# Kernel tuning notes

Measured on AMD Instinct MI355X. Metric: run time of the kernel, lower is better.

## Reference

```python
import jax, jax.numpy as jnp
import numpy as np

B, NBAND, C, T = 2, 40, 64, 1500
NUM_CODE = 1024


def setup_inputs() -> dict:
    key = jax.random.key(0)
    k1, k2 = jax.random.split(key)
    x = jax.random.normal(k1, (B, NBAND, C, T), dtype=jnp.float32)
    # layer_idx == 0 init: unit-norm codes per band
    cb = jax.random.normal(k2, (NBAND, NUM_CODE, C), dtype=jnp.float32)
    eps = jnp.finfo(jnp.float32).eps
    cb = cb / jnp.sqrt(jnp.sum(cb * cb, axis=-1, keepdims=True) + eps)
    return {"x": x, "codebook": cb}


def reference(x, codebook):
    batch, nband, nchan, time = x.shape
    num_code = codebook.shape[1]
    # x.detach().permute(0,3,1,2).view(B*T, nband, nchan)
    xd = jax.lax.stop_gradient(x).transpose(0, 3, 1, 2).reshape(batch * time, nband, nchan)
    dist = (
        jnp.sum(xd * xd, axis=-1, keepdims=True)
        + jnp.sum(codebook * codebook, axis=-1)
        - 2.0 * jnp.einsum("nbc,bkc->nbk", xd, codebook)
    )
    min_idx = jnp.argmin(dist, axis=-1)  # [BT, nband]
    # per-band gather: quantized[n, b] = codebook[b, min_idx[n, b]]
    quantized = codebook[jnp.arange(nband)[None, :], min_idx]  # [BT, nband, nchan]
    # view(B, T, nband, nchan).permute(0,2,3,1)
    return quantized.reshape(batch, time, nband, nchan).transpose(0, 2, 3, 1)
```

## Files before the change

### kernel.cpp

```cpp
#include <hip/hip_runtime.h>


#define NBAND  40
#define CH     64
#define TT     1500
#define NCODE  1024
#define MT     64
#define NTILE  24
#define PAD    68
#define THRESH 1e-3f

typedef short v8s __attribute__((ext_vector_type(8)));
typedef float v4f __attribute__((ext_vector_type(4)));

#define CBF_USHORTS ((size_t)NBAND * 32 * 8 * 64 * 8)
#define CBF_BYTES   (CBF_USHORTS * 2)
#define WS_NEEDED   (CBF_BYTES + (size_t)NBAND * NCODE * 4)

__device__ __forceinline__ unsigned short f2bf(float f) {
    unsigned u = __float_as_uint(f);
    return (unsigned short)((u + 0x7FFFu + ((u >> 16) & 1u)) >> 16);
}
__device__ __forceinline__ float bf2f(unsigned short h) {
    return __uint_as_float(((unsigned)h) << 16);
}
__device__ __forceinline__ unsigned ford(float f) {
    unsigned u = __float_as_uint(f);
    return (u & 0x80000000u) ? ~u : (u | 0x80000000u);
}
__device__ __forceinline__ unsigned long long packsk(float f, unsigned k) {
    return ((unsigned long long)ford(f) << 32) | (unsigned long long)k;
}
__device__ __forceinline__ float med3f(float a, float b, float c) {
#if __has_builtin(__builtin_amdgcn_fmed3f)
    return __builtin_amdgcn_fmed3f(a, b, c);
#else
    return fminf(fmaxf(a, b), c);
#endif
}

typedef __attribute__((address_space(1))) const unsigned char* gas_p;
typedef __attribute__((address_space(3))) unsigned char*       las_p;
__device__ __forceinline__ void async_ld16(const void* g, void* l) {
    __builtin_amdgcn_global_load_lds((gas_p)g, (las_p)l, 16, 0, 0);
}

__global__ __launch_bounds__(256)
void vq_prep(const float* __restrict__ cb,
             unsigned short* __restrict__ CBF,
             float* __restrict__ C2) {
    const int id     = blockIdx.x;
    const int v      = id >> 3;
    const int band   = (id & 7) + 8 * (v % 5);
    const int gchunk = v / 5;
    const int g      = gchunk * 4 + (threadIdx.x >> 6);
    const int lane   = threadIdx.x & 63;
    const int col    = lane & 15;
    const int quad   = lane >> 4;

    float sq[2] = {0.f, 0.f};
    #pragma unroll
    for (int l = 0; l < 4; ++l) {
        const int ni = l >> 1, ks = l & 1;
        const int code = g * 32 + ni * 16 + col;
        const int c0   = ks * 32 + quad * 8;
        const float* src = cb + ((size_t)(band * NCODE + code)) * CH + c0;
        const float4 v0 = *(const float4*)src;
        const float4 v1 = *(const float4*)(src + 4);
        const float vv[8] = {v0.x, v0.y, v0.z, v0.w, v1.x, v1.y, v1.z, v1.w};
        union { unsigned short u[8]; v8s v; } hh, ll;
        #pragma unroll
        for (int j = 0; j < 8; ++j) {
            const unsigned short h = f2bf(vv[j]);
            hh.u[j] = h;
            ll.u[j] = f2bf(vv[j] - bf2f(h));
            sq[ni] = fmaf(vv[j], vv[j], sq[ni]);
        }
        const size_t gb = (size_t)(band * 32 + g) * 8;
        *(v8s*)&CBF[(gb + l)     * 512 + lane * 8] = hh.v;
        *(v8s*)&CBF[(gb + 4 + l) * 512 + lane * 8] = ll.v;
    }
    #pragma unroll
    for (int ni = 0; ni < 2; ++ni) {
        sq[ni] += __shfl_xor(sq[ni], 16);
        sq[ni] += __shfl_xor(sq[ni], 32);
    }
    if (quad == 0) {
        C2[band * NCODE + g * 32 + col]      = sq[0];
        C2[band * NCODE + g * 32 + 16 + col] = sq[1];
    }
}

__global__ __launch_bounds__(256, 4)
void vq_main(const float* __restrict__ x,
             const float* __restrict__ cb,
             const unsigned short* __restrict__ CBF,
             const float* __restrict__ C2f,
             float* __restrict__ out) {
    __shared__ alignas(16) unsigned char SMEM[32768];
    __shared__ float c2_s[NCODE];
    __shared__ unsigned long long best_s[MT];
    __shared__ unsigned amb_s[2];
    __shared__ float xrow_s[CH];

    const int id    = blockIdx.x;
    const int v     = id >> 3;
    const int band  = (id & 7) + 8 * (v % 5);
    const int tb    = v / 5;
    const int tile  = tb % NTILE;
    const int batch = tb / NTILE;
    const int t0    = tile * MT;

    const int tid   = threadIdx.x;
    const int wave  = tid >> 6;
    const int lane  = tid & 63;
    const int quad  = lane >> 4;
    const int col   = lane & 15;
    const int thalf = wave & 1;
    const int khalf = wave >> 1;

    if (tid < 2) amb_s[tid] = 0u;
    {
        const float* src = C2f + band * NCODE;
        #pragma unroll
        for (int i = 0; i < 4; ++i) c2_s[tid + 256 * i] = src[tid + 256 * i];
    }
    {
        unsigned short* XH_s = (unsigned short*)SMEM;
        unsigned short* XL_s = XH_s + MT * PAD;
        const int c = tid & 63;
        const int g = tid >> 6;
        const float* src = x + ((size_t)(batch * NBAND + band) * CH + c) * TT + t0;
        #pragma unroll
        for (int i = 0; i < 4; ++i) {
            const int t = (g + 4 * i) * 4;
            float4 v4 = make_float4(0.f, 0.f, 0.f, 0.f);
            if (t0 + t + 3 < TT) v4 = *(const float4*)(src + t);
            const float vv[4] = {v4.x, v4.y, v4.z, v4.w};
            #pragma unroll
            for (int j = 0; j < 4; ++j) {
                const unsigned short h = f2bf(vv[j]);
                XH_s[(t + j) * PAD + c] = h;
                XL_s[(t + j) * PAD + c] = f2bf(vv[j] - bf2f(h));
            }
        }
    }
    __syncthreads();

    v8s ah[2][2], al[2][2];
    {
        unsigned short* XH_s = (unsigned short*)SMEM;
        unsigned short* XL_s = XH_s + MT * PAD;
        #pragma unroll
        for (int mi = 0; mi < 2; ++mi)
            #pragma unroll
            for (int ks = 0; ks < 2; ++ks) {
                const int off = (thalf * 32 + mi * 16 + col) * PAD + ks * 32 + quad * 8;
                ah[mi][ks] = *(const v8s*)&XH_s[off];
                al[mi][ks] = *(const v8s*)&XL_s[off];
            }
    }
    __syncthreads();

    float m1[8], m2[8];
    int   id8[8];
    #pragma unroll
    for (int i = 0; i < 8; ++i) { m1[i] = 3.4028235e38f; m2[i] = 3.4028235e38f; id8[i] = 0x7fffffff; }

    unsigned short* LBUF = (unsigned short*)SMEM;
    const unsigned short* cbase = CBF + (size_t)(band * 32) * 4096 + (size_t)lane * 8;
    const int pbase = thalf * 4;

    auto stage_round = [&](int r, int b) {
        const int group = khalf * 16 + r;
        #pragma unroll
        for (int i = 0; i < 4; ++i) {
            const int p = pbase + i;
            async_ld16(cbase + (size_t)group * 4096 + p * 512,
                       LBUF + (size_t)b * 8192 + khalf * 4096 + p * 512);
        }
    };

    stage_round(0, 0);

    for (int r = 0; r < 16; ++r) {
        __syncthreads();
        if (r + 1 < 16) stage_round(r + 1, (r + 1) & 1);

        const unsigned short* lb = LBUF + (size_t)(r & 1) * 8192 + khalf * 4096 + lane * 8;
        v4f acc[2][2];
        #pragma unroll
        for (int mi = 0; mi < 2; ++mi)
            #pragma unroll
            for (int ni = 0; ni < 2; ++ni) acc[mi][ni] = (v4f){0.f, 0.f, 0.f, 0.f};

        #pragma unroll
        for (int ks = 0; ks < 2; ++ks) {
            const v8s bh0 = *(const v8s*)(lb + (0 + ks) * 512);
            const v8s bh1 = *(const v8s*)(lb + (2 + ks) * 512);
            const v8s bl0 = *(const v8s*)(lb + (4 + ks) * 512);
            const v8s bl1 = *(const v8s*)(lb + (6 + ks) * 512);
            #pragma unroll
            for (int mi = 0; mi < 2; ++mi) {
                acc[mi][0] = __builtin_amdgcn_mfma_f32_16x16x32_bf16(ah[mi][ks], bh0, acc[mi][0], 0, 0, 0);
                acc[mi][1] = __builtin_amdgcn_mfma_f32_16x16x32_bf16(ah[mi][ks], bh1, acc[mi][1], 0, 0, 0);
            }
            #pragma unroll
            for (int mi = 0; mi < 2; ++mi) {
                acc[mi][0] = __builtin_amdgcn_mfma_f32_16x16x32_bf16(ah[mi][ks], bl0, acc[mi][0], 0, 0, 0);
                acc[mi][1] = __builtin_amdgcn_mfma_f32_16x16x32_bf16(ah[mi][ks], bl1, acc[mi][1], 0, 0, 0);
            }
            #pragma unroll
            for (int mi = 0; mi < 2; ++mi) {
                acc[mi][0] = __builtin_amdgcn_mfma_f32_16x16x32_bf16(al[mi][ks], bh0, acc[mi][0], 0, 0, 0);
                acc[mi][1] = __builtin_amdgcn_mfma_f32_16x16x32_bf16(al[mi][ks], bh1, acc[mi][1], 0, 0, 0);
            }
        }
        #pragma unroll
        for (int ni = 0; ni < 2; ++ni) {
            const int   kg  = khalf * 512 + r * 32 + ni * 16 + col;
            const float c2v = c2_s[kg];
            #pragma unroll
            for (int mi = 0; mi < 2; ++mi)
                #pragma unroll
                for (int rr = 0; rr < 4; ++rr) {
                    const int j = mi * 4 + rr;
                    const float s = fmaf(-2.f, acc[mi][ni][rr], c2v);
                    m2[j] = med3f(s, m1[j], m2[j]);
                    const bool lt = s < m1[j];
                    m1[j]  = lt ? s : m1[j];
                    id8[j] = lt ? kg : id8[j];
                }
        }
    }
    __syncthreads();

    float* RM1 = (float*)SMEM;
    float* RM2 = RM1 + MT * 32;
    int*   RI  = (int*)(RM2 + MT * 32);
    #pragma unroll
    for (int j = 0; j < 8; ++j) {
        const int t    = thalf * 32 + (j >> 2) * 16 + quad * 4 + (j & 3);
        const int slot = khalf * 16 + col;
        RM1[t * 32 + slot] = m1[j];
        RM2[t * 32 + slot] = m2[j];
        RI [t * 32 + slot] = id8[j];
    }
    __syncthreads();

    if (tid < MT) {
        const int t = tid;
        float M1 = RM1[t * 32], M2 = RM2[t * 32];
        int   I  = RI[t * 32];
        #pragma unroll 8
        for (int j = 1; j < 32; ++j) {
            const float a1 = RM1[t * 32 + j];
            const float a2 = RM2[t * 32 + j];
            const int   ai = RI [t * 32 + j];
            if (a1 < M1 || (a1 == M1 && ai < I)) { M2 = fminf(M2, M1); M1 = a1; I = ai; }
            else                                  { M2 = fminf(M2, a1); }
            M2 = fminf(M2, a2);
        }
        best_s[t] = packsk(M1, (unsigned)I);
        if ((M2 - M1) <= THRESH && t0 + t < TT)
            atomicOr(&amb_s[t >> 5], 1u << (t & 31));
    }
    __syncthreads();

    for (int t = 0; t < MT; ++t) {
        if ((amb_s[t >> 5] >> (t & 31)) & 1u) {
            if (tid < CH) xrow_s[tid] = x[((size_t)(batch * NBAND + band) * CH + tid) * TT + t0 + t];
            if (tid == CH) best_s[t] = ~0ULL;
            __syncthreads();
            #pragma unroll
            for (int i = 0; i < 4; ++i) {
                const int k = tid * 4 + i;
                const float* crow = cb + ((size_t)(band * NCODE + k)) * CH;
                float dot = 0.f, c2e = 0.f;
                #pragma unroll 8
                for (int c = 0; c < CH; ++c) {
                    const float cv = crow[c];
                    dot = fmaf(cv, xrow_s[c], dot);
                    c2e = fmaf(cv, cv, c2e);
                }
                atomicMin(&best_s[t], packsk(fmaf(-2.f, dot, c2e), (unsigned)k));
            }
            __syncthreads();
        }
    }
    __syncthreads();

    {
        float* OT = (float*)SMEM;
        #pragma unroll
        for (int rr = 0; rr < MT; rr += 4) {
            const int row = rr + wave;
            const unsigned idx = (unsigned)(best_s[row] & 0xFFFFFFFFull) & (NCODE - 1);
            OT[row * 67 + lane] = cb[((size_t)(band * NCODE + idx)) * CH + lane];
        }
        __syncthreads();
        const int tloc = tid & 63;
        const int cq   = tid >> 6;
        if (t0 + tloc < TT) {
            float* ob = out + ((size_t)(batch * NBAND + band) * CH) * TT + t0 + tloc;
            #pragma unroll
            for (int i = 0; i < 16; ++i) {
                const int c = cq * 16 + i;
                ob[(size_t)c * TT] = OT[tloc * 67 + c];
            }
        }
    }
}

#define TN 128
#define KC 128
__global__ __launch_bounds__(256, 2)
void vq_fp32_kernel(const float* __restrict__ x,
                    const float* __restrict__ cb,
                    float* __restrict__ out) {
    __shared__ float XT_s[CH * TN];
    __shared__ float CBT_s[CH * KC];
    __shared__ float c2part[256];
    const int tile = blockIdx.x, band = blockIdx.y, batch = blockIdx.z;
    const int t0 = tile * TN;
    const int tid = threadIdx.x;
    const int tx = tid & 15, ty = tid >> 4;
    {
        const int c = tid >> 2, q = tid & 3;
        const float* src = x + ((size_t)(batch * NBAND + band) * CH + c) * TT + t0;
        #pragma unroll
        for (int i = 0; i < 8; ++i) {
            const int t = q * 32 + i * 4;
            float4 v = make_float4(0.f, 0.f, 0.f, 0.f);
            if (t0 + t < TT) v = *(const float4*)(src + t);
            *(float4*)&XT_s[c * TN + t] = v;
        }
    }
    float vmin[8]; int vidx[8];
    #pragma unroll
    for (int i = 0; i < 8; ++i) { vmin[i] = 3.4e38f; vidx[i] = 0x7fffffff; }
    for (int kc = 0; kc < NCODE; kc += KC) {
        __syncthreads();
        {
            const int k = tid >> 1, ch0 = (tid & 1) * 32;
            const float* src = cb + ((size_t)(band * NCODE + kc + k)) * CH + ch0;
            float s = 0.f;
            #pragma unroll
            for (int i = 0; i < 8; ++i) {
                const float4 v = *(const float4*)(src + i * 4);
                const int c0 = ch0 + i * 4;
                CBT_s[(c0 + 0) * KC + k] = v.x; CBT_s[(c0 + 1) * KC + k] = v.y;
                CBT_s[(c0 + 2) * KC + k] = v.z; CBT_s[(c0 + 3) * KC + k] = v.w;
                s = fmaf(v.x, v.x, s); s = fmaf(v.y, v.y, s);
                s = fmaf(v.z, v.z, s); s = fmaf(v.w, v.w, s);
            }
            c2part[tid] = s;
        }
        __syncthreads();
        float acc[8][8];
        #pragma unroll
        for (int ii = 0; ii < 8; ++ii)
            #pragma unroll
            for (int jj = 0; jj < 8; ++jj) acc[ii][jj] = 0.f;
        #pragma unroll 4
        for (int c = 0; c < CH; ++c) {
            const float4 xa0 = *(const float4*)&XT_s[c * TN + tx * 4];
            const float4 xa1 = *(const float4*)&XT_s[c * TN + 64 + tx * 4];
            const float4 cv0 = *(const float4*)&CBT_s[c * KC + ty * 4];
            const float4 cv1 = *(const float4*)&CBT_s[c * KC + 64 + ty * 4];
            const float xa[8] = {xa0.x, xa0.y, xa0.z, xa0.w, xa1.x, xa1.y, xa1.z, xa1.w};
            const float cv[8] = {cv0.x, cv0.y, cv0.z, cv0.w, cv1.x, cv1.y, cv1.z, cv1.w};
            #pragma unroll
            for (int ii = 0; ii < 8; ++ii)
                #pragma unroll
                for (int jj = 0; jj < 8; ++jj) acc[ii][jj] = fmaf(xa[ii], cv[jj], acc[ii][jj]);
        }
        #pragma unroll
        for (int jj = 0; jj < 8; ++jj) {
            const int kl = (jj < 4) ? (ty * 4 + jj) : (64 + ty * 4 + (jj - 4));
            const float c2v = c2part[2 * kl] + c2part[2 * kl + 1];
            const int kglob = kc + kl;
            #pragma unroll
            for (int ii = 0; ii < 8; ++ii) {
                const float score = fmaf(-2.f, acc[ii][jj], c2v);
                if (score < vmin[ii]) { vmin[ii] = score; vidx[ii] = kglob; }
            }
        }
    }
    __syncthreads();
    float* redv = XT_s;
    int* redi = (int*)(XT_s + TN * 16);
    int* idxs = (int*)(XT_s + TN * 32);
    #pragma unroll
    for (int ii = 0; ii < 8; ++ii) {
        const int t = (ii < 4) ? (tx * 4 + ii) : (64 + tx * 4 + (ii - 4));
        redv[t * 16 + ty] = vmin[ii];
        redi[t * 16 + ty] = vidx[ii];
    }
    __syncthreads();
    if (tid < TN) {
        float bv = redv[tid * 16]; int bi = redi[tid * 16];
        #pragma unroll
        for (int j = 1; j < 16; ++j) {
            const float v = redv[tid * 16 + j]; const int id = redi[tid * 16 + j];
            if (v < bv || (v == bv && id < bi)) { bv = v; bi = id; }
        }
        idxs[tid] = bi;
    }
    __syncthreads();
    {
        const int tloc = tid & 127, chalf = tid >> 7;
        if (t0 + tloc < TT) {
            const int idx = idxs[tloc];
            const float* crow = cb + ((size_t)(band * NCODE + idx)) * CH;
            float* ob = out + ((size_t)(batch * NBAND + band) * CH) * TT + t0 + tloc;
            #pragma unroll
            for (int i = 0; i < 32; ++i) {
                const int c = chalf * 32 + i;
                ob[(size_t)c * TT] = crow[c];
            }
        }
    }
}

extern "C" void kernel_launch(void* const* d_in, const int* in_sizes, int n_in,
                              void* d_out, int out_size, void* d_ws, size_t ws_size,
                              hipStream_t stream) {
    const float* x  = (const float*)d_in[0];
    const float* cb = (const float*)d_in[1];
    float* out = (float*)d_out;
    if (ws_size >= WS_NEEDED) {
        unsigned short* CBF = (unsigned short*)d_ws;
        float* C2 = (float*)((char*)d_ws + CBF_BYTES);
        vq_prep<<<dim3(8 * 5 * 8), dim3(256), 0, stream>>>(cb, CBF, C2);
        vq_main<<<dim3(8 * 5 * NTILE * 2), dim3(256), 0, stream>>>(x, cb, CBF, C2, out);
    } else {
        dim3 grid((TT + TN - 1) / TN, NBAND, 2);
        vq_fp32_kernel<<<grid, dim3(256), 0, stream>>>(x, cb, out);
    }
}
```

Baseline: 194.2 us.

## Double time tile to 128 rows and reduce argmin with wave shuffles

Measured after the change: 215.7 us. 1.11x slower.

```diff
diff --git a/kernel.cpp b/kernel.cpp
--- a/kernel.cpp
+++ b/kernel.cpp
@@ -5,8 +5,8 @@
 #define CH     64
 #define TT     1500
 #define NCODE  1024
-#define MT     64
-#define NTILE  24
+#define MT     128
+#define NTILE  12
 #define PAD    68
 #define THRESH 1e-3f
 
@@ -27,6 +27,9 @@
 __device__ __forceinline__ unsigned ford(float f) {
     unsigned u = __float_as_uint(f);
     return (u & 0x80000000u) ? ~u : (u | 0x80000000u);
+}
+__device__ __forceinline__ float finv(unsigned u) {
+    return (u & 0x80000000u) ? __uint_as_float(u & 0x7FFFFFFFu) : __uint_as_float(~u);
 }
 __device__ __forceinline__ unsigned long long packsk(float f, unsigned k) {
     return ((unsigned long long)ford(f) << 32) | (unsigned long long)k;
@@ -91,16 +94,18 @@
     }
 }
 
-__global__ __launch_bounds__(256, 4)
+__global__ __launch_bounds__(256, 3)
 void vq_main(const float* __restrict__ x,
              const float* __restrict__ cb,
              const unsigned short* __restrict__ CBF,
              const float* __restrict__ C2f,
              float* __restrict__ out) {
-    __shared__ alignas(16) unsigned char SMEM[32768];
+    __shared__ alignas(16) unsigned char SMEM[MT * PAD * 2 * 2];
     __shared__ float c2_s[NCODE];
     __shared__ unsigned long long best_s[MT];
-    __shared__ unsigned amb_s[2];
+    __shared__ unsigned long long MB_s[MT * 2];
+    __shared__ float MS_s[MT * 2];
+    __shared__ unsigned amb_s[4];
     __shared__ float xrow_s[CH];
 
     const int id    = blockIdx.x;
@@ -119,7 +124,7 @@
     const int thalf = wave & 1;
     const int khalf = wave >> 1;
 
-    if (tid < 2) amb_s[tid] = 0u;
+    if (tid < 4) amb_s[tid] = 0u;
     {
         const float* src = C2f + band * NCODE;
         #pragma unroll
@@ -132,7 +137,7 @@
         const int g = tid >> 6;
         const float* src = x + ((size_t)(batch * NBAND + band) * CH + c) * TT + t0;
         #pragma unroll
-        for (int i = 0; i < 4; ++i) {
+        for (int i = 0; i < 8; ++i) {
             const int t = (g + 4 * i) * 4;
             float4 v4 = make_float4(0.f, 0.f, 0.f, 0.f);
             if (t0 + t + 3 < TT) v4 = *(const float4*)(src + t);
@@ -147,25 +152,25 @@
     }
     __syncthreads();
 
-    v8s ah[2][2], al[2][2];
+    v8s ah[4][2], al[4][2];
     {
         unsigned short* XH_s = (unsigned short*)SMEM;
         unsigned short* XL_s = XH_s + MT * PAD;
         #pragma unroll
-        for (int mi = 0; mi < 2; ++mi)
+        for (int mi = 0; mi < 4; ++mi)
             #pragma unroll
             for (int ks = 0; ks < 2; ++ks) {
-                const int off = (thalf * 32 + mi * 16 + col) * PAD + ks * 32 + quad * 8;
+                const int off = (thalf * 64 + mi * 16 + col) * PAD + ks * 32 + quad * 8;
                 ah[mi][ks] = *(const v8s*)&XH_s[off];
                 al[mi][ks] = *(const v8s*)&XL_s[off];
             }
     }
     __syncthreads();
 
-    float m1[8], m2[8];
-    int   id8[8];
-    #pragma unroll
-    for (int i = 0; i < 8; ++i) { m1[i] = 3.4028235e38f; m2[i] = 3.4028235e38f; id8[i] = 0x7fffffff; }
+    float m1[16], m2[16];
+    int   id16[16];
+    #pragma unroll
+    for (int i = 0; i < 16; ++i) { m1[i] = 3.4028235e38f; m2[i] = 3.4028235e38f; id16[i] = 0x7fffffff; }
 
     unsigned short* LBUF = (unsigned short*)SMEM;
     const unsigned short* cbase = CBF + (size_t)(band * 32) * 4096 + (size_t)lane * 8;
@@ -188,82 +193,73 @@
         if (r + 1 < 16) stage_round(r + 1, (r + 1) & 1);
 
         const unsigned short* lb = LBUF + (size_t)(r & 1) * 8192 + khalf * 4096 + lane * 8;
-        v4f acc[2][2];
-        #pragma unroll
-        for (int mi = 0; mi < 2; ++mi)
-            #pragma unroll
-            for (int ni = 0; ni < 2; ++ni) acc[mi][ni] = (v4f){0.f, 0.f, 0.f, 0.f};
-
-        #pragma unroll
-        for (int ks = 0; ks < 2; ++ks) {
-            const v8s bh0 = *(const v8s*)(lb + (0 + ks) * 512);
-            const v8s bh1 = *(const v8s*)(lb + (2 + ks) * 512);
-            const v8s bl0 = *(const v8s*)(lb + (4 + ks) * 512);
-            const v8s bl1 = *(const v8s*)(lb + (6 + ks) * 512);
-            #pragma unroll
-            for (int mi = 0; mi < 2; ++mi) {
-                acc[mi][0] = __builtin_amdgcn_mfma_f32_16x16x32_bf16(ah[mi][ks], bh0, acc[mi][0], 0, 0, 0);
-                acc[mi][1] = __builtin_amdgcn_mfma_f32_16x16x32_bf16(ah[mi][ks], bh1, acc[mi][1], 0, 0, 0);
-            }
-            #pragma unroll
-            for (int mi = 0; mi < 2; ++mi) {
-                acc[mi][0] = __builtin_amdgcn_mfma_f32_16x16x32_bf16(ah[mi][ks], bl0, acc[mi][0], 0, 0, 0);
-                acc[mi][1] = __builtin_amdgcn_mfma_f32_16x16x32_bf16(ah[mi][ks], bl1, acc[mi][1], 0, 0, 0);
-            }
-            #pragma unroll
-            for (int mi = 0; mi < 2; ++mi) {
-                acc[mi][0] = __builtin_amdgcn_mfma_f32_16x16x32_bf16(al[mi][ks], bh0, acc[mi][0], 0, 0, 0);
-                acc[mi][1] = __builtin_amdgcn_mfma_f32_16x16x32_bf16(al[mi][ks], bh1, acc[mi][1], 0, 0, 0);
-            }
-        }
         #pragma unroll
         for (int ni = 0; ni < 2; ++ni) {
+            v4f acc[4];
+            #pragma unroll
+            for (int mi = 0; mi < 4; ++mi) acc[mi] = (v4f){0.f, 0.f, 0.f, 0.f};
+            #pragma unroll
+            for (int ks = 0; ks < 2; ++ks) {
+                const v8s bh = *(const v8s*)(lb + (ni * 2 + ks) * 512);
+                #pragma unroll
+                for (int mi = 0; mi < 4; ++mi)
+                    acc[mi] = __builtin_amdgcn_mfma_f32_16x16x32_bf16(ah[mi][ks], bh, acc[mi], 0, 0, 0);
+                #pragma unroll
+                for (int mi = 0; mi < 4; ++mi)
+                    acc[mi] = __builtin_amdgcn_mfma_f32_16x16x32_bf16(al[mi][ks], bh, acc[mi], 0, 0, 0);
+                const v8s bl = *(const v8s*)(lb + (4 + ni * 2 + ks) * 512);
+                #pragma unroll
+                for (int mi = 0; mi < 4; ++mi)
+                    acc[mi] = __builtin_amdgcn_mfma_f32_16x16x32_bf16(ah[mi][ks], bl, acc[mi], 0, 0, 0);
+            }
             const int   kg  = khalf * 512 + r * 32 + ni * 16 + col;
             const float c2v = c2_s[kg];
             #pragma unroll
-            for (int mi = 0; mi < 2; ++mi)
+            for (int mi = 0; mi < 4; ++mi)
                 #pragma unroll
                 for (int rr = 0; rr < 4; ++rr) {
                     const int j = mi * 4 + rr;
-                    const float s = fmaf(-2.f, acc[mi][ni][rr], c2v);
+                    const float s = fmaf(-2.f, acc[mi][rr], c2v);
                     m2[j] = med3f(s, m1[j], m2[j]);
                     const bool lt = s < m1[j];
-                    m1[j]  = lt ? s : m1[j];
-                    id8[j] = lt ? kg : id8[j];
+                    m1[j]   = lt ? s : m1[j];
+                    id16[j] = lt ? kg : id16[j];
                 }
         }
     }
-    __syncthreads();
-
-    float* RM1 = (float*)SMEM;
-    float* RM2 = RM1 + MT * 32;
-    int*   RI  = (int*)(RM2 + MT * 32);
-    #pragma unroll
-    for (int j = 0; j < 8; ++j) {
-        const int t    = thalf * 32 + (j >> 2) * 16 + quad * 4 + (j & 3);
-        const int slot = khalf * 16 + col;
-        RM1[t * 32 + slot] = m1[j];
-        RM2[t * 32 + slot] = m2[j];
-        RI [t * 32 + slot] = id8[j];
+
+    #pragma unroll
+    for (int j = 0; j < 16; ++j) {
+        float b1 = m1[j], b2 = m2[j];
+        int   bi = id16[j];
+        #pragma unroll
+        for (int d = 1; d < 16; d <<= 1) {
+            const float o1 = __shfl_xor(b1, d);
+            const float o2 = __shfl_xor(b2, d);
+            const int   oi = __shfl_xor(bi, d);
+            b2 = fminf(fminf(b2, o2), fmaxf(b1, o1));
+            const bool take = (o1 < b1) || (o1 == b1 && oi < bi);
+            b1 = take ? o1 : b1;
+            bi = take ? oi : bi;
+        }
+        if (col == 0) {
+            const int t = thalf * 64 + (j >> 2) * 16 + quad * 4 + (j & 3);
+            MB_s[t * 2 + khalf] = packsk(b1, (unsigned)bi);
+            MS_s[t * 2 + khalf] = b2;
+        }
     }
     __syncthreads();
 
     if (tid < MT) {
-        const int t = tid;
-        float M1 = RM1[t * 32], M2 = RM2[t * 32];
-        int   I  = RI[t * 32];
-        #pragma unroll 8
-        for (int j = 1; j < 32; ++j) {
-            const float a1 = RM1[t * 32 + j];
-            const float a2 = RM2[t * 32 + j];
-            const int   ai = RI [t * 32 + j];
-            if (a1 < M1 || (a1 == M1 && ai < I)) { M2 = fminf(M2, M1); M1 = a1; I = ai; }
-            else                                  { M2 = fminf(M2, a1); }
-            M2 = fminf(M2, a2);
-        }
-        best_s[t] = packsk(M1, (unsigned)I);
-        if ((M2 - M1) <= THRESH && t0 + t < TT)
-            atomicOr(&amb_s[t >> 5], 1u << (t & 31));
+        const unsigned long long b0 = MB_s[tid * 2];
+        const unsigned long long b1 = MB_s[tid * 2 + 1];
+        const unsigned long long bmin = (b0 < b1) ? b0 : b1;
+        const unsigned long long bmax = (b0 < b1) ? b1 : b0;
+        const float M1 = finv((unsigned)(bmin >> 32));
+        const float M2 = fminf(fminf(MS_s[tid * 2], MS_s[tid * 2 + 1]), finv((unsigned)(bmax >> 32)));
+        best_s[tid] = bmin;
+        if ((M2 - M1) <= THRESH && t0 + tid < TT)
+            atomicOr(&amb_s[tid >> 5], 1u << (tid & 31));
     }
     __syncthreads();
 
@@ -299,13 +295,13 @@
             OT[row * 67 + lane] = cb[((size_t)(band * NCODE + idx)) * CH + lane];
         }
         __syncthreads();
-        const int tloc = tid & 63;
-        const int cq   = tid >> 6;
+        const int tloc  = tid & 127;
+        const int chalf = tid >> 7;
         if (t0 + tloc < TT) {
             float* ob = out + ((size_t)(batch * NBAND + band) * CH) * TT + t0 + tloc;
             #pragma unroll
-            for (int i = 0; i < 16; ++i) {
-                const int c = cq * 16 + i;
+            for (int i = 0; i < 32; ++i) {
+                const int c = chalf * 32 + i;
                 ob[(size_t)c * TT] = OT[tloc * 67 + c];
             }
         }
```
